# Kernel tuning notes

Measured on AMD Instinct MI355X. Metric: run time of the kernel, lower is better.

Reference implementation:

```python
import jax, jax.numpy as jnp
import numpy as np

K = 7          # median window size
PAD = (K - 1) // 2  # same padding with stride 1


def setup_inputs() -> dict:
    key = jax.random.key(0)
    x = jax.random.uniform(key, (8, 3, 512, 512), dtype=jnp.float32)
    return {"x": x}


def _median_pool_hardtanh(x):
    B, C, H, W = x.shape
    # reflect pad, same as F.pad(..., mode='reflect') with (pl,pr,pt,pb)=(3,3,3,3)
    xp = jnp.pad(x, ((0, 0), (0, 0), (PAD, PAD), (PAD, PAD)), mode='reflect')
    # Gather the 49 shifted views of the padded image (fixed small loop over
    # kernel offsets, vectorized over B,C,H,W). Shape: [B,C,H,W,49]
    patches = jnp.stack(
        [xp[:, :, i:i + H, j:j + W] for i in range(K) for j in range(K)],
        axis=-1,
    )
    # torch .median(dim=-1) over an odd count (49) equals the true median
    med = jnp.median(patches, axis=-1)
    # Hardtanh(min_val=0, max_val=1)
    return jnp.clip(med, 0.0, 1.0)


def reference(x):
    return _median_pool_hardtanh(x)
```

## Files before the change

kernel.cpp:

```cpp
#include <hip/hip_runtime.h>

#define DEV __device__ __forceinline__

template <int N> struct V { float v[N == 0 ? 1 : N]; };

template <int M, int N>
DEV V<M + N> mrg(V<M> a, V<N> b) {
    V<M + N> o;
    if constexpr (M == 0) {
#pragma unroll
        for (int i = 0; i < N; ++i) o.v[i] = b.v[i];
    } else if constexpr (N == 0) {
#pragma unroll
        for (int i = 0; i < M; ++i) o.v[i] = a.v[i];
    } else if constexpr (M == 1 && N == 1) {
        o.v[0] = fminf(a.v[0], b.v[0]);
        o.v[1] = fmaxf(a.v[0], b.v[0]);
    } else if constexpr ((M & 1) && (N & 1)) {
        constexpr int AE = (M + 1) / 2, AO = M / 2, BE = (N + 1) / 2, BO = N / 2;
        V<AE> ae; V<AO> ao; V<BE> be; V<BO> bo;
#pragma unroll
        for (int i = 0; i < AE; ++i) ae.v[i] = a.v[2 * i];
#pragma unroll
        for (int i = 0; i < AO; ++i) ao.v[i] = a.v[2 * i + 1];
#pragma unroll
        for (int i = 0; i < BE; ++i) be.v[i] = b.v[2 * i];
#pragma unroll
        for (int i = 0; i < BO; ++i) bo.v[i] = b.v[2 * i + 1];
        V<AE + BO> E = mrg<AE, BO>(ae, bo);
        V<AO + BE> O = mrg<AO, BE>(ao, be);
        constexpr int P = AE + BO;
#pragma unroll
        for (int i = 0; i < P; ++i) {
            o.v[2 * i] = fminf(E.v[i], O.v[i]);
            o.v[2 * i + 1] = fmaxf(E.v[i], O.v[i]);
        }
    } else {
        constexpr int AE = (M + 1) / 2, AO = M / 2, BE = (N + 1) / 2, BO = N / 2;
        V<AE> ae; V<AO> ao; V<BE> be; V<BO> bo;
#pragma unroll
        for (int i = 0; i < AE; ++i) ae.v[i] = a.v[2 * i];
#pragma unroll
        for (int i = 0; i < AO; ++i) ao.v[i] = a.v[2 * i + 1];
#pragma unroll
        for (int i = 0; i < BE; ++i) be.v[i] = b.v[2 * i];
#pragma unroll
        for (int i = 0; i < BO; ++i) bo.v[i] = b.v[2 * i + 1];
        V<AE + BE> E = mrg<AE, BE>(ae, be);
        V<AO + BO> O = mrg<AO, BO>(ao, bo);
        constexpr int CEn = AE + BE, COn = AO + BO;
        o.v[0] = E.v[0];
#pragma unroll
        for (int i = 0; i < COn; ++i) {
            if (i + 1 < CEn) {
                o.v[2 * i + 1] = fminf(O.v[i], E.v[i + 1]);
                o.v[2 * i + 2] = fmaxf(O.v[i], E.v[i + 1]);
            } else {
                o.v[2 * i + 1] = O.v[i];
            }
        }
    }
    return o;
}

DEV void ce(float& a, float& b) {
    float lo = fminf(a, b);
    b = fmaxf(a, b);
    a = lo;
}

DEV V<7> sort7(V<7> x) {
    ce(x.v[1], x.v[2]); ce(x.v[0], x.v[2]); ce(x.v[0], x.v[1]);
    ce(x.v[3], x.v[4]); ce(x.v[5], x.v[6]); ce(x.v[3], x.v[5]);
    ce(x.v[4], x.v[6]); ce(x.v[4], x.v[5]);
    V<3> a; a.v[0] = x.v[0]; a.v[1] = x.v[1]; a.v[2] = x.v[2];
    V<4> b; b.v[0] = x.v[3]; b.v[1] = x.v[4]; b.v[2] = x.v[5]; b.v[3] = x.v[6];
    return mrg<3, 4>(a, b);
}

DEV float sel24(V<28> Q, V<21> F) {
    float m = Q.v[24];
#pragma unroll
    for (int i = 4; i < 25; ++i) m = fminf(m, fmaxf(Q.v[i - 1], F.v[24 - i]));
    return m;
}

static constexpr int W = 512, H = 512, PLANE = W * H;

__global__ __launch_bounds__(256, 1) void median7_hardtanh_kernel(
    const float* __restrict__ in, float* __restrict__ out) {
    int local = (int)threadIdx.x;
    int tx = local & 127;
    int ry = local >> 7;
    int r = blockIdx.x * 2 + ry;
    int y = r & (H - 1);
    int p = r >> 9;
    const float* img = in + (size_t)p * PLANE;
    int x0 = tx * 4;

    int rows[7];
#pragma unroll
    for (int i = 0; i < 7; ++i) {
        int t = y + i - 3;
        t = (t < 0) ? -t : t;
        t = (t > H - 1) ? 2 * (H - 1) - t : t;
        rows[i] = t << 9;
    }

    V<7> c0, c1, c2, c3, c4, c5, c6, c7, c8, c9;
    if (x0 >= 4 && x0 <= W - 8) {
#pragma unroll
        for (int i = 0; i < 7; ++i) {
            const float* rp = img + rows[i] + x0;
            float4 L = *reinterpret_cast<const float4*>(rp - 4);
            float4 C = *reinterpret_cast<const float4*>(rp);
            float4 R = *reinterpret_cast<const float4*>(rp + 4);
            c0.v[i] = L.y; c1.v[i] = L.z; c2.v[i] = L.w;
            c3.v[i] = C.x; c4.v[i] = C.y; c5.v[i] = C.z; c6.v[i] = C.w;
            c7.v[i] = R.x; c8.v[i] = R.y; c9.v[i] = R.z;
        }
    } else {
        int cols[10];
#pragma unroll
        for (int j = 0; j < 10; ++j) {
            int u = x0 + j - 3;
            u = (u < 0) ? -u : u;
            u = (u > W - 1) ? 2 * (W - 1) - u : u;
            cols[j] = u;
        }
#pragma unroll
        for (int i = 0; i < 7; ++i) {
            const float* rp = img + rows[i];
            c0.v[i] = rp[cols[0]]; c1.v[i] = rp[cols[1]]; c2.v[i] = rp[cols[2]];
            c3.v[i] = rp[cols[3]]; c4.v[i] = rp[cols[4]]; c5.v[i] = rp[cols[5]];
            c6.v[i] = rp[cols[6]]; c7.v[i] = rp[cols[7]]; c8.v[i] = rp[cols[8]];
            c9.v[i] = rp[cols[9]];
        }
    }

    c0 = sort7(c0); c1 = sort7(c1); c2 = sort7(c2); c3 = sort7(c3);
    c4 = sort7(c4); c5 = sort7(c5); c6 = sort7(c6); c7 = sort7(c7);
    c8 = sort7(c8); c9 = sort7(c9);

    V<28> Q = mrg<14, 14>(mrg<7, 7>(c3, c4), mrg<7, 7>(c5, c6));
    V<14> P12 = mrg<7, 7>(c1, c2);
    V<14> P78 = mrg<7, 7>(c7, c8);

    float m0 = sel24(Q, mrg<14, 7>(P12, c0));
    float m1 = sel24(Q, mrg<14, 7>(P12, c7));
    float m2 = sel24(Q, mrg<14, 7>(P78, c2));
    float m3 = sel24(Q, mrg<14, 7>(P78, c9));

    float4 o;
    o.x = fminf(fmaxf(m0, 0.0f), 1.0f);
    o.y = fminf(fmaxf(m1, 0.0f), 1.0f);
    o.z = fminf(fmaxf(m2, 0.0f), 1.0f);
    o.w = fminf(fmaxf(m3, 0.0f), 1.0f);
    *reinterpret_cast<float4*>(out + (size_t)r * W + x0) = o;
}

extern "C" void kernel_launch(void* const* d_in, const int* in_sizes, int n_in,
                              void* d_out, int out_size, void* d_ws, size_t ws_size,
                              hipStream_t stream) {
    const float* x = (const float*)d_in[0];
    float* outp = (float*)d_out;
    int rows_total = out_size / W;
    int blocks = rows_total / 2;
    median7_hardtanh_kernel<<<blocks, 256, 0, stream>>>(x, outp);
}
```

Measured before the change: 132.3 us.

## Stage column loads and sorts to cut register pressure, use med3 and tree min

Result: slower. 137.5 us (+4.0%).

```diff
diff --git a/kernel.cpp b/kernel.cpp
--- a/kernel.cpp
+++ b/kernel.cpp
@@ -70,33 +70,41 @@
 }
 
 DEV V<7> sort7(V<7> x) {
-    ce(x.v[1], x.v[2]); ce(x.v[0], x.v[2]); ce(x.v[0], x.v[1]);
-    ce(x.v[3], x.v[4]); ce(x.v[5], x.v[6]); ce(x.v[3], x.v[5]);
-    ce(x.v[4], x.v[6]); ce(x.v[4], x.v[5]);
-    V<3> a; a.v[0] = x.v[0]; a.v[1] = x.v[1]; a.v[2] = x.v[2];
-    V<4> b; b.v[0] = x.v[3]; b.v[1] = x.v[4]; b.v[2] = x.v[5]; b.v[3] = x.v[6];
-    return mrg<3, 4>(a, b);
+    float a = x.v[0], b = x.v[1], c = x.v[2];
+    V<3> s3;
+    s3.v[0] = fminf(fminf(a, b), c);
+    s3.v[1] = __builtin_amdgcn_fmed3f(a, b, c);
+    s3.v[2] = fmaxf(fmaxf(a, b), c);
+    ce(x.v[3], x.v[4]); ce(x.v[5], x.v[6]);
+    ce(x.v[3], x.v[5]); ce(x.v[4], x.v[6]); ce(x.v[4], x.v[5]);
+    V<4> s4;
+    s4.v[0] = x.v[3]; s4.v[1] = x.v[4]; s4.v[2] = x.v[5]; s4.v[3] = x.v[6];
+    return mrg<3, 4>(s3, s4);
 }
 
-DEV float sel24(V<28> Q, V<21> F) {
-    float m = Q.v[24];
+DEV float sel24(const V<28>& Q, const V<21>& F) {
+    float t[22];
+    t[21] = Q.v[24];
 #pragma unroll
-    for (int i = 4; i < 25; ++i) m = fminf(m, fmaxf(Q.v[i - 1], F.v[24 - i]));
-    return m;
+    for (int i = 4; i < 25; ++i) t[i - 4] = fmaxf(Q.v[i - 1], F.v[24 - i]);
+#pragma unroll
+    for (int i = 0; i < 11; ++i) t[i] = fminf(t[i], t[i + 11]);
+#pragma unroll
+    for (int i = 0; i < 5; ++i) t[i] = fminf(t[i], t[i + 6]);
+#pragma unroll
+    for (int i = 0; i < 3; ++i) t[i] = fminf(t[i], t[i + 3]);
+    return fminf(fminf(t[0], t[1]), t[2]);
 }
 
 static constexpr int W = 512, H = 512, PLANE = W * H;
 
-__global__ __launch_bounds__(256, 1) void median7_hardtanh_kernel(
+__global__ __launch_bounds__(128, 1) void median7_hardtanh_kernel(
     const float* __restrict__ in, float* __restrict__ out) {
-    int local = (int)threadIdx.x;
-    int tx = local & 127;
-    int ry = local >> 7;
-    int r = blockIdx.x * 2 + ry;
+    int r = blockIdx.x;
     int y = r & (H - 1);
     int p = r >> 9;
     const float* img = in + (size_t)p * PLANE;
-    int x0 = tx * 4;
+    int x0 = (int)threadIdx.x << 2;
 
     int rows[7];
 #pragma unroll
@@ -107,48 +115,60 @@
         rows[i] = t << 9;
     }
 
-    V<7> c0, c1, c2, c3, c4, c5, c6, c7, c8, c9;
-    if (x0 >= 4 && x0 <= W - 8) {
+    int cl0 = x0 - 3; cl0 = cl0 < 0 ? -cl0 : cl0;
+    int cl1 = x0 - 2; cl1 = cl1 < 0 ? -cl1 : cl1;
+    int cl2 = x0 - 1; cl2 = cl2 < 0 ? -cl2 : cl2;
+    int cr0 = x0 + 4; cr0 = cr0 > W - 1 ? 2 * (W - 1) - cr0 : cr0;
+    int cr1 = x0 + 5; cr1 = cr1 > W - 1 ? 2 * (W - 1) - cr1 : cr1;
+    int cr2 = x0 + 6; cr2 = cr2 > W - 1 ? 2 * (W - 1) - cr2 : cr2;
+
+    V<7> c3, c4, c5, c6;
 #pragma unroll
-        for (int i = 0; i < 7; ++i) {
-            const float* rp = img + rows[i] + x0;
-            float4 L = *reinterpret_cast<const float4*>(rp - 4);
-            float4 C = *reinterpret_cast<const float4*>(rp);
-            float4 R = *reinterpret_cast<const float4*>(rp + 4);
-            c0.v[i] = L.y; c1.v[i] = L.z; c2.v[i] = L.w;
-            c3.v[i] = C.x; c4.v[i] = C.y; c5.v[i] = C.z; c6.v[i] = C.w;
-            c7.v[i] = R.x; c8.v[i] = R.y; c9.v[i] = R.z;
-        }
-    } else {
-        int cols[10];
+    for (int i = 0; i < 7; ++i) {
+        float4 C = *reinterpret_cast<const float4*>(img + rows[i] + x0);
+        c3.v[i] = C.x; c4.v[i] = C.y; c5.v[i] = C.z; c6.v[i] = C.w;
+    }
+    c3 = sort7(c3); c4 = sort7(c4); c5 = sort7(c5); c6 = sort7(c6);
+    V<28> Q = mrg<14, 14>(mrg<7, 7>(c3, c4), mrg<7, 7>(c5, c6));
+    __builtin_amdgcn_sched_barrier(0);
+
+    V<7> c1, c2;
 #pragma unroll
-        for (int j = 0; j < 10; ++j) {
-            int u = x0 + j - 3;
-            u = (u < 0) ? -u : u;
-            u = (u > W - 1) ? 2 * (W - 1) - u : u;
-            cols[j] = u;
-        }
+    for (int i = 0; i < 7; ++i) {
+        const float* rp = img + rows[i];
+        c1.v[i] = rp[cl1];
+        c2.v[i] = rp[cl2];
+    }
+    c1 = sort7(c1); c2 = sort7(c2);
+    V<14> P12 = mrg<7, 7>(c1, c2);
+    __builtin_amdgcn_sched_barrier(0);
+
+    V<7> c0;
 #pragma unroll
-        for (int i = 0; i < 7; ++i) {
-            const float* rp = img + rows[i];
-            c0.v[i] = rp[cols[0]]; c1.v[i] = rp[cols[1]]; c2.v[i] = rp[cols[2]];
-            c3.v[i] = rp[cols[3]]; c4.v[i] = rp[cols[4]]; c5.v[i] = rp[cols[5]];
-            c6.v[i] = rp[cols[6]]; c7.v[i] = rp[cols[7]]; c8.v[i] = rp[cols[8]];
-            c9.v[i] = rp[cols[9]];
-        }
-    }
+    for (int i = 0; i < 7; ++i) c0.v[i] = img[rows[i] + cl0];
+    c0 = sort7(c0);
+    float m0 = sel24(Q, mrg<14, 7>(P12, c0));
+    __builtin_amdgcn_sched_barrier(0);
 
-    c0 = sort7(c0); c1 = sort7(c1); c2 = sort7(c2); c3 = sort7(c3);
-    c4 = sort7(c4); c5 = sort7(c5); c6 = sort7(c6); c7 = sort7(c7);
-    c8 = sort7(c8); c9 = sort7(c9);
+    V<7> c7;
+#pragma unroll
+    for (int i = 0; i < 7; ++i) c7.v[i] = img[rows[i] + cr0];
+    c7 = sort7(c7);
+    float m1 = sel24(Q, mrg<14, 7>(P12, c7));
+    __builtin_amdgcn_sched_barrier(0);
 
-    V<28> Q = mrg<14, 14>(mrg<7, 7>(c3, c4), mrg<7, 7>(c5, c6));
-    V<14> P12 = mrg<7, 7>(c1, c2);
+    V<7> c8;
+#pragma unroll
+    for (int i = 0; i < 7; ++i) c8.v[i] = img[rows[i] + cr1];
+    c8 = sort7(c8);
     V<14> P78 = mrg<7, 7>(c7, c8);
+    float m2 = sel24(Q, mrg<14, 7>(P78, c2));
+    __builtin_amdgcn_sched_barrier(0);
 
-    float m0 = sel24(Q, mrg<14, 7>(P12, c0));
-    float m1 = sel24(Q, mrg<14, 7>(P12, c7));
-    float m2 = sel24(Q, mrg<14, 7>(P78, c2));
+    V<7> c9;
+#pragma unroll
+    for (int i = 0; i < 7; ++i) c9.v[i] = img[rows[i] + cr2];
+    c9 = sort7(c9);
     float m3 = sel24(Q, mrg<14, 7>(P78, c9));
 
     float4 o;
@@ -165,6 +185,5 @@
     const float* x = (const float*)d_in[0];
     float* outp = (float*)d_out;
     int rows_total = out_size / W;
-    int blocks = rows_total / 2;
-    median7_hardtanh_kernel<<<blocks, 256, 0, stream>>>(x, outp);
+    median7_hardtanh_kernel<<<rows_total, 128, 0, stream>>>(x, outp);
 }
```
